# Optimization experiments

Measured on AMD Instinct MI355X. Metric: run time of the kernel, lower is better.

## Reference

```python
import jax, jax.numpy as jnp
import numpy as np

T, B, D_IN, D_H = 512, 256, 128, 128


def setup_inputs() -> dict:
    key = jax.random.key(0)
    ks = jax.random.split(key, 13)
    D = D_IN + D_H
    s = 1.0 / np.sqrt(D)  # torch nn.Linear default init bound
    inp = {"inputs": jax.random.normal(ks[0], (T, B, D_IN), jnp.float32)}
    for i, n in enumerate(["forget", "input", "update", "output"]):
        inp[f"W_{n}"] = jax.random.uniform(ks[1 + 3 * i], (2, D), jnp.float32, -s, s)
        inp[f"b_{n}"] = jax.random.uniform(ks[2 + 3 * i], (2,), jnp.float32, -s, s)
        inp[f"theta_{n}"] = jax.random.uniform(ks[3 + 3 * i], (2,), jnp.float32, 0.0, 2.0 * np.pi)
    return inp


def _qgate(comb, W, b, theta):
    # SamplerQNN analytic form (2 qubits):
    #   RY(x0)RY(th0) on wire0, RY(x1)RY(th1) on wire1, CNOT(0,1), measure <Z0>.
    #   Consecutive RYs compose; Z0 commutes with CNOT (wire0 is control),
    #   so QLayer output = <Z0> = cos(x0 + th0). Wire-1 params do not affect it.
    z0 = comb @ W[0] + b[0]  # first row of the 2-dim Linear projection: (B,)
    return jnp.cos(z0 + theta[0])


def reference(inputs, W_forget, b_forget, theta_forget, W_input, b_input, theta_input,
              W_update, b_update, theta_update, W_output, b_output, theta_output):
    Bsz = inputs.shape[1]
    h0 = jnp.zeros((Bsz, D_H), inputs.dtype)
    c0 = jnp.zeros((Bsz, D_H), inputs.dtype)

    def step(carry, x_t):
        hx, cx = carry
        comb = jnp.concatenate([x_t, hx], axis=1)  # (B, D_IN + D_H)
        # per-batch scalar gate activations, broadcast over hidden dim
        f = jax.nn.sigmoid(_qgate(comb, W_forget, b_forget, theta_forget))[:, None]
        i = jax.nn.sigmoid(_qgate(comb, W_input, b_input, theta_input))[:, None]
        g = jnp.tanh(_qgate(comb, W_update, b_update, theta_update))[:, None]
        o = jax.nn.sigmoid(_qgate(comb, W_output, b_output, theta_output))[:, None]
        cx = f * cx + i * g
        hx = o * jnp.tanh(cx)
        return (hx, cx), hx

    (hx, cx), outputs = jax.lax.scan(step, (h0, c0), inputs)
    return outputs, hx, cx
```

## Files before the change

kernel.cpp:

```cpp
#include <hip/hip_runtime.h>
#include <hip/hip_bf16.h>


constexpr int T = 512;
constexpr int Bsz = 256;
constexpr int R = T * Bsz;
constexpr int CH = 128;
constexpr int NCH = T / CH;
constexpr int MEMB = 2016;
constexpr int GRID = 32 + MEMB;
constexpr float INV2PI = 0.15915494309189535f;

typedef float f4v __attribute__((ext_vector_type(4)));

__device__ __forceinline__ float tanh9(float c) {
    const float y  = c * c;
    const float y2 = y * y;
    const float lo  = fmaf(y, -0.321470f, 0.999168f);
    const float hi  = fmaf(y, 0.0016407f, -0.0199491f);
    const float mid = fmaf(y, hi, 0.101498f);
    return c * fmaf(y2, mid, lo);
}

template<int CTRL>
__device__ __forceinline__ float dppq(float x) {
    return __builtin_bit_cast(float,
        __builtin_amdgcn_mov_dpp(__builtin_bit_cast(int, x), CTRL, 0xF, 0xF, true));
}

__device__ __forceinline__ float wsum(const float* __restrict__ W, int lane) {
    float s = W[128 + lane] + W[192 + lane];
#pragma unroll
    for (int off = 32; off; off >>= 1) s += __shfl_xor(s, off, 64);
    return s;
}

__global__ __launch_bounds__(256) void pipe_kernel(
    const int k,
    const float* __restrict__ x,
    const float* __restrict__ Wf, const float* __restrict__ bf, const float* __restrict__ tf,
    const float* __restrict__ Wi, const float* __restrict__ bi, const float* __restrict__ ti,
    const float* __restrict__ Wu, const float* __restrict__ bu, const float* __restrict__ tu,
    const float* __restrict__ Wo, const float* __restrict__ bo, const float* __restrict__ to_,
    float4* __restrict__ xz, float* __restrict__ hscan,
    float* __restrict__ hstate, float* __restrict__ cstate,
    float4* __restrict__ out4)
{
    const int tid = threadIdx.x;

    if (blockIdx.x < 32) {
        if (k < 0 || k >= NCH) return;
        __shared__ float4 zb4[CH * 8];
        const int bb = blockIdx.x * 8;
        const int cb = k * CH;

#pragma unroll
        for (int it = 0; it < CH * 8 / 256; ++it) {
            const int j = it * 256 + tid;
            zb4[j] = xz[(size_t)(cb + (j >> 3)) * Bsz + bb + (j & 7)];
        }

        const int l = tid & 63;
        const float swf = wsum(Wf, l) * INV2PI;
        const float swi = wsum(Wi, l) * INV2PI;
        const float swu = wsum(Wu, l) * INV2PI;
        const float swo = wsum(Wo, l) * INV2PI;

        __syncthreads();
        if (tid >= 32) return;

        const int q = tid & 3;
        const int batch = bb + (tid >> 2);

        const float sw = (q == 0) ? swf : (q == 1) ? swi : (q == 2) ? swu : swo;

        const bool tq = (q == 2);
        const float K0 = tq ? 0.0f       : 0.5f;
        const float K1 = tq ? 0.999318f  : 0.249976f;
        const float K3 = tq ? -0.319476f : -0.0206916f;
        const float K5 = tq ? 0.08315f   : 0.00188244f;

        const float* zl = (const float*)zb4 + tid;
        float* hp = hscan + (size_t)cb * Bsz + batch;

        float h, c;
        if (k == 0) { h = 0.0f; c = 0.0f; }
        else        { h = hstate[batch]; c = cstate[batch]; }

#define HSTEP(Y)                                                   \
    {                                                              \
        const float u  = fmaf(h, sw, (Y));                         \
        const float v  = __builtin_amdgcn_cosf(u);                 \
        const float v2 = v * v;                                    \
        const float t1 = fmaf(v2, K5, K3);                         \
        const float p  = fmaf(v2, t1, K1);                         \
        const float gown = fmaf(v, p, K0);                         \
        const float f  = dppq<0x00>(gown);                         \
        const float i  = dppq<0x55>(gown);                         \
        const float g_ = dppq<0xAA>(gown);                         \
        const float o  = dppq<0xFF>(gown);                         \
        c = fmaf(f, c, i * g_);                                    \
        h = o * tanh9(c);                                          \
        *hp = h;                                                   \
        hp += Bsz;                                                 \
    }

        float p0 = zl[0 * 32], p1 = zl[1 * 32], p2 = zl[2 * 32], p3 = zl[3 * 32];
        float p4 = zl[4 * 32], p5 = zl[5 * 32], p6 = zl[6 * 32], p7 = zl[7 * 32];

        for (int tb = 0; tb < CH - 8; tb += 8) {
            const float* zn = zl + (size_t)(tb + 8) * 32;
            const float n0 = zn[0 * 32];
            const float n1 = zn[1 * 32];
            const float n2 = zn[2 * 32];
            const float n3 = zn[3 * 32];
            const float n4 = zn[4 * 32];
            const float n5 = zn[5 * 32];
            const float n6 = zn[6 * 32];
            const float n7 = zn[7 * 32];
            HSTEP(p0); HSTEP(p1); HSTEP(p2); HSTEP(p3);
            HSTEP(p4); HSTEP(p5); HSTEP(p6); HSTEP(p7);
            p0 = n0; p1 = n1; p2 = n2; p3 = n3;
            p4 = n4; p5 = n5; p6 = n6; p7 = n7;
        }
        HSTEP(p0); HSTEP(p1); HSTEP(p2); HSTEP(p3);
        HSTEP(p4); HSTEP(p5); HSTEP(p6); HSTEP(p7);
#undef HSTEP

        hstate[batch] = h;
        cstate[batch] = c;
        return;
    }

    const int mb   = blockIdx.x - 32;
    const int wv   = tid >> 6;
    const int lane = tid & 63;
    const int hl   = lane & 31;
    const int half = lane >> 5;

    if (k + 1 < NCH) {
        const float4 wfv = ((const float4*)Wf)[hl];
        const float4 wiv = ((const float4*)Wi)[hl];
        const float4 wuv = ((const float4*)Wu)[hl];
        const float4 wov = ((const float4*)Wo)[hl];
        const float cf = bf[0] + tf[0];
        const float ci = bi[0] + ti[0];
        const float cu = bu[0] + tu[0];
        const float co = bo[0] + to_[0];

        const int slab = (k + 1) * CH * Bsz;
        for (int p = mb * 4 + wv; p < CH * Bsz / 2; p += MEMB * 4) {
            const int row = slab + 2 * p + half;
            const float4 xv = *(const float4*)(x + (size_t)row * 128 + hl * 4);

            float pf = xv.x * wfv.x + xv.y * wfv.y + xv.z * wfv.z + xv.w * wfv.w;
            float pi = xv.x * wiv.x + xv.y * wiv.y + xv.z * wiv.z + xv.w * wiv.w;
            float pu = xv.x * wuv.x + xv.y * wuv.y + xv.z * wuv.z + xv.w * wuv.w;
            float po = xv.x * wov.x + xv.y * wov.y + xv.z * wov.z + xv.w * wov.w;

#pragma unroll
            for (int off = 16; off; off >>= 1) {
                pf += __shfl_xor(pf, off, 64);
                pi += __shfl_xor(pi, off, 64);
                pu += __shfl_xor(pu, off, 64);
                po += __shfl_xor(po, off, 64);
            }
            if (hl == 0) {
                xz[row] = make_float4((pf + cf) * INV2PI, (pi + ci) * INV2PI,
                                      (pu + cu) * INV2PI, (po + co) * INV2PI);
            }
        }
    }

    if (k >= 1 && k <= NCH) {
        const int slabr = (k - 1) * CH * Bsz;
        for (int j = mb * 256 + tid; j < CH * Bsz * 32; j += MEMB * 256) {
            const int row = slabr + (j >> 5);
            const float v = hscan[row];
            const f4v val = {v, v, v, v};
            __builtin_nontemporal_store(val, (f4v*)&out4[(size_t)row * 32 + (j & 31)]);
        }
    }

    if (k == NCH) {
        for (int j = mb * 256 + tid; j < 2 * Bsz * 32; j += MEMB * 256) {
            const int kind = j >> 13;
            const int r    = (j >> 5) & 255;
            const int col  = j & 31;
            const float v = kind ? cstate[r] : hscan[(size_t)(T - 1) * Bsz + r];
            const f4v val = {v, v, v, v};
            __builtin_nontemporal_store(
                val, (f4v*)&out4[((size_t)R + (size_t)kind * Bsz + r) * 32 + col]);
        }
    }
}

extern "C" void kernel_launch(void* const* d_in, const int* in_sizes, int n_in,
                              void* d_out, int out_size, void* d_ws, size_t ws_size,
                              hipStream_t stream)
{
    const float* x  = (const float*)d_in[0];
    const float* Wf = (const float*)d_in[1];
    const float* bf = (const float*)d_in[2];
    const float* tf = (const float*)d_in[3];
    const float* Wi = (const float*)d_in[4];
    const float* bi = (const float*)d_in[5];
    const float* ti = (const float*)d_in[6];
    const float* Wu = (const float*)d_in[7];
    const float* bu = (const float*)d_in[8];
    const float* tu = (const float*)d_in[9];
    const float* Wo = (const float*)d_in[10];
    const float* bo = (const float*)d_in[11];
    const float* to_ = (const float*)d_in[12];

    float* ws     = (float*)d_ws;
    float4* xz    = (float4*)ws;
    float* hscan  = ws + 4 * R;
    float* hstate = ws + 5 * R;
    float* cstate = ws + 5 * R + Bsz;

    for (int k = -1; k <= NCH; ++k) {
        pipe_kernel<<<GRID, 256, 0, stream>>>(
            k, x, Wf, bf, tf, Wi, bi, ti, Wu, bu, tu, Wo, bo, to_,
            xz, hscan, hstate, cstate, (float4*)d_out);
    }
}
```

Baseline: 60.21 us.

## Use uneven chunk sizes in the pipelined scan and shorten the recurrence dependency chain

```diff
diff --git a/kernel.cpp b/kernel.cpp
--- a/kernel.cpp
+++ b/kernel.cpp
@@ -5,10 +5,9 @@
 constexpr int T = 512;
 constexpr int Bsz = 256;
 constexpr int R = T * Bsz;
-constexpr int CH = 128;
-constexpr int NCH = T / CH;
 constexpr int MEMB = 2016;
 constexpr int GRID = 32 + MEMB;
+constexpr int MAXCH = 192;
 constexpr float INV2PI = 0.15915494309189535f;
 
 typedef float f4v __attribute__((ext_vector_type(4)));
@@ -36,7 +35,9 @@
 }
 
 __global__ __launch_bounds__(256) void pipe_kernel(
-    const int k,
+    const int xz_t0, const int xz_len,
+    const int sc_t0, const int sc_len,
+    const int wr_t0, const int wr_len, const int do_tails,
     const float* __restrict__ x,
     const float* __restrict__ Wf, const float* __restrict__ bf, const float* __restrict__ tf,
     const float* __restrict__ Wi, const float* __restrict__ bi, const float* __restrict__ ti,
@@ -49,16 +50,12 @@
     const int tid = threadIdx.x;
 
     if (blockIdx.x < 32) {
-        if (k < 0 || k >= NCH) return;
-        __shared__ float4 zb4[CH * 8];
+        if (sc_len == 0) return;
+        __shared__ float4 zb4[MAXCH * 8];
         const int bb = blockIdx.x * 8;
-        const int cb = k * CH;
-
-#pragma unroll
-        for (int it = 0; it < CH * 8 / 256; ++it) {
-            const int j = it * 256 + tid;
-            zb4[j] = xz[(size_t)(cb + (j >> 3)) * Bsz + bb + (j & 7)];
-        }
+
+        for (int j = tid; j < sc_len * 8; j += 256)
+            zb4[j] = xz[(size_t)(sc_t0 + (j >> 3)) * Bsz + bb + (j & 7)];
 
         const int l = tid & 63;
         const float swf = wsum(Wf, l) * INV2PI;
@@ -81,15 +78,16 @@
         const float K5 = tq ? 0.08315f   : 0.00188244f;
 
         const float* zl = (const float*)zb4 + tid;
-        float* hp = hscan + (size_t)cb * Bsz + batch;
+        float* hp = hscan + (size_t)sc_t0 * Bsz + batch;
 
         float h, c;
-        if (k == 0) { h = 0.0f; c = 0.0f; }
-        else        { h = hstate[batch]; c = cstate[batch]; }
+        if (sc_t0 == 0) { h = 0.0f; c = 0.0f; }
+        else            { h = hstate[batch]; c = cstate[batch]; }
+        float tc = h, os = sw;
 
 #define HSTEP(Y)                                                   \
     {                                                              \
-        const float u  = fmaf(h, sw, (Y));                         \
+        const float u  = fmaf(tc, os, (Y));                        \
         const float v  = __builtin_amdgcn_cosf(u);                 \
         const float v2 = v * v;                                    \
         const float t1 = fmaf(v2, K5, K3);                         \
@@ -99,8 +97,10 @@
         const float i  = dppq<0x55>(gown);                         \
         const float g_ = dppq<0xAA>(gown);                         \
         const float o  = dppq<0xFF>(gown);                         \
-        c = fmaf(f, c, i * g_);                                    \
-        h = o * tanh9(c);                                          \
+        c  = fmaf(f, c, i * g_);                                   \
+        tc = tanh9(c);                                             \
+        os = o * sw;                                               \
+        h  = o * tc;                                               \
         *hp = h;                                                   \
         hp += Bsz;                                                 \
     }
@@ -108,7 +108,7 @@
         float p0 = zl[0 * 32], p1 = zl[1 * 32], p2 = zl[2 * 32], p3 = zl[3 * 32];
         float p4 = zl[4 * 32], p5 = zl[5 * 32], p6 = zl[6 * 32], p7 = zl[7 * 32];
 
-        for (int tb = 0; tb < CH - 8; tb += 8) {
+        for (int tb = 0; tb + 8 < sc_len; tb += 8) {
             const float* zn = zl + (size_t)(tb + 8) * 32;
             const float n0 = zn[0 * 32];
             const float n1 = zn[1 * 32];
@@ -138,7 +138,7 @@
     const int hl   = lane & 31;
     const int half = lane >> 5;
 
-    if (k + 1 < NCH) {
+    if (xz_len > 0) {
         const float4 wfv = ((const float4*)Wf)[hl];
         const float4 wiv = ((const float4*)Wi)[hl];
         const float4 wuv = ((const float4*)Wu)[hl];
@@ -148,8 +148,9 @@
         const float cu = bu[0] + tu[0];
         const float co = bo[0] + to_[0];
 
-        const int slab = (k + 1) * CH * Bsz;
-        for (int p = mb * 4 + wv; p < CH * Bsz / 2; p += MEMB * 4) {
+        const int slab = xz_t0 * Bsz;
+        const int npairs = xz_len * Bsz / 2;
+        for (int p = mb * 4 + wv; p < npairs; p += MEMB * 4) {
             const int row = slab + 2 * p + half;
             const float4 xv = *(const float4*)(x + (size_t)row * 128 + hl * 4);
 
@@ -172,9 +173,10 @@
         }
     }
 
-    if (k >= 1 && k <= NCH) {
-        const int slabr = (k - 1) * CH * Bsz;
-        for (int j = mb * 256 + tid; j < CH * Bsz * 32; j += MEMB * 256) {
+    if (wr_len > 0) {
+        const int slabr = wr_t0 * Bsz;
+        const int total = wr_len * Bsz * 32;
+        for (int j = mb * 256 + tid; j < total; j += MEMB * 256) {
             const int row = slabr + (j >> 5);
             const float v = hscan[row];
             const f4v val = {v, v, v, v};
@@ -182,7 +184,7 @@
         }
     }
 
-    if (k == NCH) {
+    if (do_tails) {
         for (int j = mb * 256 + tid; j < 2 * Bsz * 32; j += MEMB * 256) {
             const int kind = j >> 13;
             const int r    = (j >> 5) & 255;
@@ -219,9 +221,18 @@
     float* hstate = ws + 5 * R;
     float* cstate = ws + 5 * R + Bsz;
 
-    for (int k = -1; k <= NCH; ++k) {
+    static const int c0[4] = {0, 64, 256, 448};
+    static const int cl[4] = {64, 192, 192, 64};
+    for (int i = 0; i < 6; ++i) {
+        const int xi = i,     has_x = (i < 4);
+        const int si = i - 1, has_s = (si >= 0 && si < 4);
+        const int wi = i - 2, has_w = (wi >= 0 && wi < 4);
         pipe_kernel<<<GRID, 256, 0, stream>>>(
-            k, x, Wf, bf, tf, Wi, bi, ti, Wu, bu, tu, Wo, bo, to_,
+            has_x ? c0[xi] : 0, has_x ? cl[xi] : 0,
+            has_s ? c0[si] : 0, has_s ? cl[si] : 0,
+            has_w ? c0[wi] : 0, has_w ? cl[wi] : 0,
+            (i == 5) ? 1 : 0,
+            x, Wf, bf, tf, Wi, bi, ti, Wu, bu, tu, Wo, bo, to_,
             xz, hscan, hstate, cstate, (float4*)d_out);
     }
 }
```

Result: slower. 63.25 us (+5.1%).
